# Kernel optimization log

Measured on AMD Instinct MI355X. Metric: run time of the kernel, lower is better.

The kernel has to match this reference:

```python
import jax, jax.numpy as jnp
import numpy as np

H = 128
NG, NS, NP = 50000, 20000, 30000
NUM_PC_FEATURES = 5
EPS = 1e-12


def seg_sum(x, idx, n):
    return jax.ops.segment_sum(x, idx, num_segments=n)


def seg_mean(x, idx, n):
    s = seg_sum(x, idx, n)
    cnt = seg_sum(jnp.ones((x.shape[0],), x.dtype), idx, n)
    return s / jnp.maximum(cnt, 1.0)[:, None]


def gcn_norm(row, col, n, add_self_loops):
    deg = seg_sum(jnp.ones(row.shape, jnp.float32), col, n)
    if add_self_loops:
        deg = deg + 1.0
    dinv = jnp.where(deg > 0, deg ** -0.5, 0.0)
    return dinv[row] * dinv[col], dinv


def tag_conv(x, row, col, n, Ws, b):
    # TAGConv: out = sum_k (A_hat^k x) W_k + b, symmetric norm, no self loops
    norm, _ = gcn_norm(row, col, n, False)
    out = x @ Ws[0]
    h = x
    for k in range(1, Ws.shape[0]):
        h = seg_sum(norm[:, None] * h[row], col, n)
        out = out + h @ Ws[k]
    return out + b


def rgcn_conv(x, row, col, etype, n, W, root, b):
    # RGCNConv: per-relation mean aggregation + root transform
    h = jnp.einsum('nc,rcd->rnd', x, W)  # [R, N, H]
    msg = h[etype, row]                  # [E, H]
    cnt = jnp.zeros((n, W.shape[0]), x.dtype).at[col, etype].add(1.0)
    w = 1.0 / jnp.maximum(cnt[col, etype], 1.0)
    return seg_sum(msg * w[:, None], col, n) + x @ root + b


def gcn_layer(x, row, col, n, W, b):
    # GCNConv: self loops + symmetric normalization
    xW = x @ W
    norm, dinv = gcn_norm(row, col, n, True)
    return seg_sum(norm[:, None] * xW[row], col, n) + (dinv ** 2)[:, None] * xW + b


def sage_conv(xs, xd, row, col, nd, lw, lb, rw):
    # SAGEConv with mean aggregation, root weight, L2 output normalization
    m = seg_mean(xs[row], col, nd)
    out = m @ lw + lb + xd @ rw
    nrm = jnp.maximum(jnp.linalg.norm(out, axis=-1, keepdims=True), EPS)
    return out / nrm


def setup_inputs() -> dict:
    key = jax.random.key(0)
    ks = iter(jax.random.split(key, 64))

    def nrm(shape):
        return jax.random.normal(next(ks), shape, jnp.float32) * 0.05

    def edges(ns, nd, e):
        return jnp.stack([jax.random.randint(next(ks), (e,), 0, ns, jnp.int32),
                          jax.random.randint(next(ks), (e,), 0, nd, jnp.int32)])

    return dict(
        game_x=nrm((NG, 7)),
        state_x=nrm((NS, 6)),
        pc_x=nrm((NP, NUM_PC_FEATURES)),
        edge_index_v_v=edges(NG, NG, 500000),
        edge_type_v_v=jax.random.randint(next(ks), (500000,), 0, 3, jnp.int32),
        edge_index_history_v_s=edges(NG, NS, 300000),
        edge_attr_history_v_s=nrm((300000, 2)),
        edge_index_in_v_s=edges(NG, NS, 300000),
        edge_index_s_s=edges(NS, NS, 200000),
        edge_index_pc_pc=edges(NP, NP, 300000),
        edge_index_pc_state=edges(NP, NS, 200000),
        edge_index_state_pc=edges(NS, NP, 100000),
        tag10_w=nrm((4, 7, H)), tag10_b=nrm((H,)),
        rgcn_w=nrm((3, H, H)), rgcn_root=nrm((H, H)), rgcn_b=nrm((H,)),
        gcn1_w=nrm((NUM_PC_FEATURES, H)), gcn1_b=nrm((H,)),
        gcn2_w=nrm((H, H)), gcn2_b=nrm((H,)),
        rg_key_w=nrm((6, H)), rg_key_b=nrm((H,)),
        rg_query_w=nrm((H, H)), rg_query_b=nrm((H,)),
        rg_value_w=nrm((H, H)), rg_value_b=nrm((H,)),
        rg_edge_w=nrm((2, H)), rg_skip_w=nrm((6, H)), rg_b=nrm((H,)),
        sage32_lw=nrm((H, H)), sage32_lb=nrm((H,)), sage32_rw=nrm((H, H)),
        sage4_lw=nrm((H, H)), sage4_lb=nrm((H,)), sage4_rw=nrm((H, H)),
        sage42_lw=nrm((H, H)), sage42_lb=nrm((H,)), sage42_rw=nrm((H, H)),
        pcs_lw=nrm((H, H)), pcs_lb=nrm((H,)), pcs_rw=nrm((H, H)),
        tag2_w=nrm((3, H, H)), tag2_b=nrm((H,)),
        sage5_lw=nrm((H, H)), sage5_lb=nrm((H,)), sage5_rw=nrm((H, H)),
        lin_w=nrm((H, 32)), lin_b=nrm((32,)),
        linl_w=nrm((32, 1)), linl_b=nrm((1,)),
    )


def reference(game_x, state_x, pc_x, edge_index_v_v, edge_type_v_v,
              edge_index_history_v_s, edge_attr_history_v_s, edge_index_in_v_s,
              edge_index_s_s, edge_index_pc_pc, edge_index_pc_state, edge_index_state_pc,
              tag10_w, tag10_b, rgcn_w, rgcn_root, rgcn_b,
              gcn1_w, gcn1_b, gcn2_w, gcn2_b,
              rg_key_w, rg_key_b, rg_query_w, rg_query_b, rg_value_w, rg_value_b,
              rg_edge_w, rg_skip_w, rg_b,
              sage32_lw, sage32_lb, sage32_rw,
              sage4_lw, sage4_lb, sage4_rw,
              sage42_lw, sage42_lb, sage42_rw,
              pcs_lw, pcs_lb, pcs_rw,
              tag2_w, tag2_b,
              sage5_lw, sage5_lb, sage5_rw,
              lin_w, lin_b, linl_w, linl_b):
    relu = jax.nn.relu
    rvv, cvv = edge_index_v_v[0], edge_index_v_v[1]
    g = relu(tag_conv(game_x, rvv, cvv, NG, tag10_w, tag10_b))
    g = relu(rgcn_conv(g, rvv, cvv, edge_type_v_v, NG, rgcn_w, rgcn_root, rgcn_b))
    rp, cp = edge_index_pc_pc[0], edge_index_pc_pc[1]
    p = relu(gcn_layer(pc_x, rp, cp, NP, gcn1_w, gcn1_b))
    p = relu(gcn_layer(p, rp, cp, NP, gcn2_w, gcn2_b))
    rh, ch = edge_index_history_v_s[0], edge_index_history_v_s[1]
    # ResGatedGraphConv((game, state), H, edge_dim=2)
    kk = state_x @ rg_key_w + rg_key_b
    q = g @ rg_query_w + rg_query_b
    v = g @ rg_value_w + rg_value_b
    e = edge_attr_history_v_s @ rg_edge_w
    eta = jax.nn.sigmoid(kk[ch] + q[rh] + e)
    s = relu(seg_sum(eta * v[rh], ch, NS) + state_x @ rg_skip_w + rg_b)
    s = relu(sage_conv(g, s, rh, ch, NS, sage32_lw, sage32_lb, sage32_rw))
    ri, ci = edge_index_in_v_s[0], edge_index_in_v_s[1]
    s = relu(sage_conv(g, s, ri, ci, NS, sage4_lw, sage4_lb, sage4_rw))
    s = relu(sage_conv(g, s, ri, ci, NS, sage42_lw, sage42_lb, sage42_rw))
    rps, cps = edge_index_pc_state[0], edge_index_pc_state[1]
    s = relu(sage_conv(p, s, rps, cps, NS, pcs_lw, pcs_lb, pcs_rw))
    rs, cs = edge_index_s_s[0], edge_index_s_s[1]
    s = relu(tag_conv(s, rs, cs, NS, tag2_w, tag2_b))
    s = relu(sage_conv(s, s, rs, cs, NS, sage5_lw, sage5_lb, sage5_rw))
    s = relu(s @ lin_w + lin_b)
    return jax.nn.log_softmax(s @ linl_w + linl_b, axis=0)
```

## Files before the change

kernel.cpp:

```cpp
#include <hip/hip_runtime.h>
#include <cstdint>

#define H 128
static const int NG = 50000, NS = 20000, NP = 30000;

#define TG_RELU 2
#define TG_NORM 4
#define TG_OUTBF16 8

#define CSR_CHUNK 8192

typedef __attribute__((ext_vector_type(8))) short bf16x8;
typedef __attribute__((ext_vector_type(4))) float f32x4;

static inline int nblk(long long n) { return (int)((n + 255) / 256); }

__device__ inline unsigned short f2b(float f) {
  unsigned int u = __float_as_uint(f);
  u += 0x7FFFu + ((u >> 16) & 1u);
  return (unsigned short)(u >> 16);
}
__device__ inline float b2f(unsigned short u) {
  return __uint_as_float(((unsigned int)u) << 16);
}

struct Seg6 {
  const int* col[6];
  const int* row[6];
  const int* et0;
  int nodeoff[7];
  int edgeoff[7];
  int mode[6];
  float addself[6];
  int hasdinv[6];
};

__global__ __launch_bounds__(256) void k_hist(Seg6 sg, int EE, int* __restrict__ table) {
  __shared__ int h[512];
  int tid = threadIdx.x, blk = blockIdx.x;
  h[tid] = 0; h[tid + 256] = 0;
  __syncthreads();
  int e0 = blk * CSR_CHUNK, e1 = min(EE, e0 + CSR_CHUNK);
  for (int e = e0 + tid; e < e1; e += 256) {
    int gi = 0;
    while (e >= sg.edgeoff[gi + 1]) gi++;
    int le = e - sg.edgeoff[gi];
    int gn = sg.nodeoff[gi] + sg.col[gi][le];
    atomicAdd(&h[gn >> 9], 1);
  }
  __syncthreads();
  table[blk * 512 + tid] = h[tid];
  table[blk * 512 + tid + 256] = h[tid + 256];
}

__global__ void k_scanT(int* __restrict__ table, int nblkA, int* __restrict__ coarseOff) {
  int b = threadIdx.x;
  int s = 0;
  for (int k = 0; k < nblkA; k++) s += table[k * 512 + b];
  __shared__ int cs[512];
  cs[b] = s;
  __syncthreads();
  for (int off = 1; off < 512; off <<= 1) {
    int v = cs[b];
    int u = (b >= off) ? cs[b - off] : 0;
    __syncthreads();
    cs[b] = v + u;
    __syncthreads();
  }
  int excl = (b > 0) ? cs[b - 1] : 0;
  coarseOff[b] = excl;
  if (b == 511) coarseOff[512] = cs[511];
  int run = excl;
  for (int k = 0; k < nblkA; k++) {
    int t = table[k * 512 + b];
    table[k * 512 + b] = run;
    run += t;
  }
}

__global__ __launch_bounds__(256) void k_scatterA(Seg6 sg, int EE, const int* __restrict__ table,
                                                  uint2* __restrict__ tmp) {
  __shared__ int cur[512];
  int tid = threadIdx.x, blk = blockIdx.x;
  cur[tid] = table[blk * 512 + tid];
  cur[tid + 256] = table[blk * 512 + tid + 256];
  __syncthreads();
  int e0 = blk * CSR_CHUNK, e1 = min(EE, e0 + CSR_CHUNK);
  for (int e = e0 + tid; e < e1; e += 256) {
    int gi = 0;
    while (e >= sg.edgeoff[gi + 1]) gi++;
    int le = e - sg.edgeoff[gi];
    int gn = sg.nodeoff[gi] + sg.col[gi][le];
    int m = sg.mode[gi];
    int pay;
    if (m == 2) pay = le;
    else {
      pay = sg.row[gi][le];
      if (m == 1) pay |= sg.et0[le] << 16;
    }
    int pos = atomicAdd(&cur[gn >> 9], 1);
    tmp[pos] = make_uint2((unsigned)gn, (unsigned)pay);
  }
}

__global__ __launch_bounds__(256) void k_localCSR(const uint2* __restrict__ tmp,
                                                  const int* __restrict__ coarseOff,
                                                  Seg6 sg, int NN, int EE, int B,
                                                  int* __restrict__ rowptr,
                                                  int* __restrict__ eidx,
                                                  float* __restrict__ dinv) {
  int b = blockIdx.x, tid = threadIdx.x;
  int base = b * 512;
  int nNodes = min(512, NN - base);
  int beg = coarseOff[b], end = coarseOff[b + 1];
  __shared__ int cnt[512];
  __shared__ int off[512];
  __shared__ int ps[256];
  cnt[tid] = 0; cnt[tid + 256] = 0;
  __syncthreads();
  for (int j = beg + tid; j < end; j += 256)
    atomicAdd(&cnt[tmp[j].x - base], 1);
  __syncthreads();
  int a = cnt[2 * tid], bb = cnt[2 * tid + 1];
  ps[tid] = a + bb;
  __syncthreads();
  for (int o = 1; o < 256; o <<= 1) {
    int v = ps[tid];
    int u = (tid >= o) ? ps[tid - o] : 0;
    __syncthreads();
    ps[tid] = v + u;
    __syncthreads();
  }
  int excl = (tid > 0) ? ps[tid - 1] : 0;
  off[2 * tid] = excl;
  off[2 * tid + 1] = excl + a;
  __syncthreads();
  for (int i = tid; i < nNodes; i += 256) {
    int gid = base + i;
    rowptr[gid] = beg + off[i];
    int gi = 0;
    while (gid >= sg.nodeoff[gi + 1]) gi++;
    if (sg.hasdinv[gi]) {
      float d = (float)cnt[i] + sg.addself[gi];
      dinv[gid] = (d > 0.f) ? rsqrtf(d) : 0.f;
    }
  }
  if (b == B - 1 && tid == 0) rowptr[NN] = EE;
  __syncthreads();
  for (int j = beg + tid; j < end; j += 256) {
    uint2 p = tmp[j];
    int pos = beg + atomicAdd(&off[p.x - base], 1);
    eidx[pos] = (int)p.y;
  }
}

struct PackD { const float* src; int Ksrc; int Kdst; };
struct Pack17 { PackD d[17]; int koff[18]; };

__global__ void k_pack(Pack17 p, unsigned short* __restrict__ Wt, int totalRows) {
  int t = blockIdx.x * blockDim.x + threadIdx.x;
  if (t >= totalRows * 128) return;
  int gk = t >> 7, n = t & 127;
  int w = 0;
  while (gk >= p.koff[w + 1]) w++;
  int k = gk - p.koff[w];
  float v = (k < p.d[w].Ksrc) ? p.d[w].src[(size_t)k * 128 + n] : 0.f;
  Wt[(size_t)p.koff[w] * 128 + (size_t)n * p.d[w].Kdst + k] = f2b(v);
}

__global__ void k_gather_mean(const unsigned short* __restrict__ src, const int* __restrict__ eidx,
                              const int* __restrict__ rowptr, const int* __restrict__ remap,
                              unsigned short* __restrict__ out) {
  int c = blockIdx.x, h = threadIdx.x;
  int beg = rowptr[c], end = rowptr[c + 1];
  __shared__ int si[128];
  float acc = 0.f;
  for (int j0 = beg; j0 < end; j0 += 128) {
    int nn = min(128, end - j0);
    __syncthreads();
    if (h < nn) {
      int e = eidx[j0 + h];
      si[h] = remap ? remap[e] : e;
    }
    __syncthreads();
    int t = 0;
    for (; t + 4 <= nn; t += 4) {
      float a0 = b2f(src[(size_t)si[t] * H + h]);
      float a1 = b2f(src[(size_t)si[t + 1] * H + h]);
      float a2 = b2f(src[(size_t)si[t + 2] * H + h]);
      float a3 = b2f(src[(size_t)si[t + 3] * H + h]);
      acc += (a0 + a1) + (a2 + a3);
    }
    for (; t < nn; t++) acc += b2f(src[(size_t)si[t] * H + h]);
  }
  int cnt = end - beg;
  out[(size_t)c * H + h] = f2b(acc * (1.f / (float)(cnt > 0 ? cnt : 1)));
}

__global__ void k_gather_rel3(const unsigned short* __restrict__ src, const int* __restrict__ eidx,
                              const int* __restrict__ rowptr, unsigned short* __restrict__ G3) {
  int c = blockIdx.x, h = threadIdx.x;
  int beg = rowptr[c], end = rowptr[c + 1];
  __shared__ int si[128];
  float a0 = 0.f, a1 = 0.f, a2 = 0.f;
  int c0 = 0, c1 = 0, c2 = 0;
  for (int j0 = beg; j0 < end; j0 += 128) {
    int nn = min(128, end - j0);
    __syncthreads();
    if (h < nn) si[h] = eidx[j0 + h];
    __syncthreads();
    for (int t = 0; t < nn; t++) {
      int pk = si[t];
      int rel = pk >> 16;
      float val = b2f(src[(size_t)(pk & 0xFFFF) * H + h]);
      if (rel == 0) { a0 += val; c0++; }
      else if (rel == 1) { a1 += val; c1++; }
      else { a2 += val; c2++; }
    }
  }
  size_t base = (size_t)c * 384;
  G3[base + h] = f2b(a0 * (1.f / (float)(c0 > 0 ? c0 : 1)));
  G3[base + 128 + h] = f2b(a1 * (1.f / (float)(c1 > 0 ? c1 : 1)));
  G3[base + 256 + h] = f2b(a2 * (1.f / (float)(c2 > 0 ? c2 : 1)));
}

__global__ void k_gather_norm(const unsigned short* __restrict__ src, int ldS, int offS,
                              const int* __restrict__ eidx, const int* __restrict__ rowptr,
                              const float* __restrict__ dinv, const unsigned short* __restrict__ selfX,
                              const float* __restrict__ bias, unsigned short* __restrict__ out,
                              int ldD, int offD, int relu) {
  int c = blockIdx.x, h = threadIdx.x;
  int beg = rowptr[c], end = rowptr[c + 1];
  __shared__ int si[128];
  __shared__ float sw[128];
  float acc = 0.f;
  for (int j0 = beg; j0 < end; j0 += 128) {
    int nn = min(128, end - j0);
    __syncthreads();
    if (h < nn) {
      int r = eidx[j0 + h];
      si[h] = r;
      sw[h] = dinv[r];
    }
    __syncthreads();
    int t = 0;
    for (; t + 4 <= nn; t += 4) {
      float a0 = sw[t] * b2f(src[(size_t)si[t] * ldS + offS + h]);
      float a1 = sw[t + 1] * b2f(src[(size_t)si[t + 1] * ldS + offS + h]);
      float a2 = sw[t + 2] * b2f(src[(size_t)si[t + 2] * ldS + offS + h]);
      float a3 = sw[t + 3] * b2f(src[(size_t)si[t + 3] * ldS + offS + h]);
      acc += (a0 + a1) + (a2 + a3);
    }
    for (; t < nn; t++) acc += sw[t] * b2f(src[(size_t)si[t] * ldS + offS + h]);
  }
  float dc = dinv[c];
  float o = acc * dc;
  if (selfX) o += dc * dc * b2f(selfX[(size_t)c * H + h]);
  if (bias) o += bias[h];
  if (relu) o = fmaxf(o, 0.f);
  out[(size_t)c * ldD + offD + h] = f2b(o);
}

__global__ void k_gather_norm7(const unsigned short* __restrict__ src, int ldS, int offS,
                               const int* __restrict__ eidx, const int* __restrict__ rowptr,
                               const float* __restrict__ dinv, unsigned short* __restrict__ dst,
                               int ldD, int offD) {
  int c = blockIdx.x;
  int t = threadIdx.x;
  int f = t & 7, j = t >> 3;
  int beg = rowptr[c], end = rowptr[c + 1];
  __shared__ int si[64];
  __shared__ float sw[64];
  __shared__ float red[8][8];
  float acc = 0.f;
  for (int j0 = beg; j0 < end; j0 += 64) {
    int nn = min(64, end - j0);
    __syncthreads();
    if (t < nn) {
      int r = eidx[j0 + t] & 0xFFFF;
      si[t] = r;
      sw[t] = dinv[r];
    }
    __syncthreads();
    if (f < 7)
      for (int u = j; u < nn; u += 8) acc += sw[u] * b2f(src[(size_t)si[u] * ldS + offS + f]);
  }
  red[j][f] = acc;
  __syncthreads();
  if (j == 0 && f < 7) {
    float s = 0.f;
    for (int u = 0; u < 8; u++) s += red[u][f];
    dst[(size_t)c * ldD + offD + f] = f2b(s * dinv[c]);
  }
}

__global__ void k_resgated_gather(const unsigned short* __restrict__ kk,
                                  const unsigned short* __restrict__ q,
                                  const unsigned short* __restrict__ v,
                                  const float* __restrict__ ea,
                                  const float* __restrict__ We, const int* __restrict__ rh,
                                  const int* __restrict__ eidx, const int* __restrict__ rowptr,
                                  const float* __restrict__ sx, const float* __restrict__ Wsk,
                                  const float* __restrict__ rgb, unsigned short* __restrict__ out) {
  int c = blockIdx.x, h = threadIdx.x;
  int beg = rowptr[c], end = rowptr[c + 1];
  __shared__ int sr[64];
  __shared__ float se0[64], se1[64];
  float kload = b2f(kk[(size_t)c * H + h]);
  float we0 = We[h], we1 = We[H + h];
  float acc = 0.f;
  for (int j0 = beg; j0 < end; j0 += 64) {
    int nn = min(64, end - j0);
    __syncthreads();
    if (h < nn) {
      int e = eidx[j0 + h];
      sr[h] = rh[e];
      se0[h] = ea[2 * e];
      se1[h] = ea[2 * e + 1];
    }
    __syncthreads();
    for (int t = 0; t < nn; t++) {
      int r = sr[t];
      float x = kload + b2f(q[(size_t)r * H + h]) + se0[t] * we0 + se1[t] * we1;
      float eta = 1.f / (1.f + __expf(-x));
      acc += eta * b2f(v[(size_t)r * H + h]);
    }
  }
  float skip = rgb[h];
#pragma unroll
  for (int f = 0; f < 6; f++) skip = fmaf(sx[c * 6 + f], Wsk[f * H + h], skip);
  out[(size_t)c * H + h] = f2b(fmaxf(acc + skip, 0.f));
}

__global__ void k_copy7b(const float* __restrict__ src, unsigned short* __restrict__ dst, int n) {
  long long t = (long long)blockIdx.x * blockDim.x + threadIdx.x;
  int i = (int)(t >> 3), f = (int)(t & 7);
  if (i < n && f < 7) dst[(size_t)i * 32 + f] = f2b(src[(size_t)i * 7 + f]);
}

__global__ void k_gemm128b(const float* __restrict__ X, const float* __restrict__ W,
                           const float* __restrict__ b, unsigned short* __restrict__ out,
                           int M, int K) {
  long long t = (long long)blockIdx.x * blockDim.x + threadIdx.x;
  if (t >= (long long)M * H) return;
  int i = (int)(t >> 7), h = (int)(t & 127);
  float acc = b ? b[h] : 0.f;
  const float* x = X + (long long)i * K;
  for (int k = 0; k < K; k++) acc = fmaf(x[k], W[k * H + h], acc);
  out[t] = f2b(acc);
}

__global__ __launch_bounds__(256) void k_mgemm(const unsigned short* __restrict__ X1, int ldX1, int K1,
                                               const unsigned short* __restrict__ W1t,
                                               const unsigned short* __restrict__ X2, int ldX2, int K2,
                                               const unsigned short* __restrict__ W2t,
                                               const float* __restrict__ bias,
                                               void* __restrict__ Cv, long ldC,
                                               int M, int flags) {
  __shared__ unsigned short Als[64 * 40];
  __shared__ unsigned short Bls[128 * 40];
  __shared__ float rs[2][64];
  int tid = threadIdx.x;
  int lane = tid & 63, wv = tid >> 6;
  int m = lane & 15, q = lane >> 4;
  int rbase = (wv & 1) * 32;
  int cbase = (wv >> 1) * 64;
  int blockRow = blockIdx.x * 64;
  int sr = tid >> 2, skc = (tid & 3) * 8;
  f32x4 acc[2][4];
#pragma unroll
  for (int a = 0; a < 2; a++)
#pragma unroll
    for (int b = 0; b < 4; b++) acc[a][b] = (f32x4){0.f, 0.f, 0.f, 0.f};

  int Ktot = K1 + K2;
  for (int k0 = 0; k0 < Ktot; k0 += 32) {
    const unsigned short* Xb;
    const unsigned short* Wt_;
    int kr, ldx, Kw;
    if (k0 < K1) { Xb = X1; Wt_ = W1t; kr = k0; ldx = ldX1; Kw = K1; }
    else { Xb = X2; Wt_ = W2t; kr = k0 - K1; ldx = ldX2; Kw = K2; }
    __syncthreads();
    {
      int gr = blockRow + sr;
      bf16x8 xv = (bf16x8){0, 0, 0, 0, 0, 0, 0, 0};
      if (gr < M) xv = *(const bf16x8*)(Xb + (size_t)gr * ldx + kr + skc);
      *(bf16x8*)&Als[sr * 40 + skc] = xv;
    }
#pragma unroll
    for (int it = 0; it < 2; it++) {
      int fid = it * 256 + tid;
      int n = fid >> 2, kc = (fid & 3) * 8;
      *(bf16x8*)&Bls[n * 40 + kc] = *(const bf16x8*)(Wt_ + (size_t)n * Kw + kr + kc);
    }
    __syncthreads();
    bf16x8 a0 = *(const bf16x8*)&Als[(rbase + m) * 40 + q * 8];
    bf16x8 a1 = *(const bf16x8*)&Als[(rbase + 16 + m) * 40 + q * 8];
    bf16x8 b0 = *(const bf16x8*)&Bls[(cbase + m) * 40 + q * 8];
    bf16x8 b1 = *(const bf16x8*)&Bls[(cbase + 16 + m) * 40 + q * 8];
    bf16x8 b2 = *(const bf16x8*)&Bls[(cbase + 32 + m) * 40 + q * 8];
    bf16x8 b3 = *(const bf16x8*)&Bls[(cbase + 48 + m) * 40 + q * 8];
    acc[0][0] = __builtin_amdgcn_mfma_f32_16x16x32_bf16(a0, b0, acc[0][0], 0, 0, 0);
    acc[0][1] = __builtin_amdgcn_mfma_f32_16x16x32_bf16(a0, b1, acc[0][1], 0, 0, 0);
    acc[0][2] = __builtin_amdgcn_mfma_f32_16x16x32_bf16(a0, b2, acc[0][2], 0, 0, 0);
    acc[0][3] = __builtin_amdgcn_mfma_f32_16x16x32_bf16(a0, b3, acc[0][3], 0, 0, 0);
    acc[1][0] = __builtin_amdgcn_mfma_f32_16x16x32_bf16(a1, b0, acc[1][0], 0, 0, 0);
    acc[1][1] = __builtin_amdgcn_mfma_f32_16x16x32_bf16(a1, b1, acc[1][1], 0, 0, 0);
    acc[1][2] = __builtin_amdgcn_mfma_f32_16x16x32_bf16(a1, b2, acc[1][2], 0, 0, 0);
    acc[1][3] = __builtin_amdgcn_mfma_f32_16x16x32_bf16(a1, b3, acc[1][3], 0, 0, 0);
  }
  float ov[2][4][4];
  float bcol[4] = {0.f, 0.f, 0.f, 0.f};
  if (bias) {
#pragma unroll
    for (int j = 0; j < 4; j++) bcol[j] = bias[cbase + j * 16 + m];
  }
#pragma unroll
  for (int a = 0; a < 2; a++)
#pragma unroll
    for (int j = 0; j < 4; j++)
#pragma unroll
      for (int i = 0; i < 4; i++) ov[a][j][i] = acc[a][j][i] + bcol[j];

  if (flags & TG_NORM) {
#pragma unroll
    for (int a = 0; a < 2; a++)
#pragma unroll
      for (int i = 0; i < 4; i++) {
        float p = 0.f;
#pragma unroll
        for (int j = 0; j < 4; j++) p = fmaf(ov[a][j][i], ov[a][j][i], p);
        p += __shfl_xor(p, 1);
        p += __shfl_xor(p, 2);
        p += __shfl_xor(p, 4);
        p += __shfl_xor(p, 8);
        if (m == 0) rs[wv >> 1][rbase + a * 16 + q * 4 + i] = p;
      }
    __syncthreads();
#pragma unroll
    for (int a = 0; a < 2; a++)
#pragma unroll
      for (int i = 0; i < 4; i++) {
        int ridx = rbase + a * 16 + q * 4 + i;
        float s = rs[0][ridx] + rs[1][ridx];
        float f = 1.f / fmaxf(sqrtf(s), 1e-12f);
#pragma unroll
        for (int j = 0; j < 4; j++) ov[a][j][i] = fmaxf(ov[a][j][i] * f, 0.f);
      }
  } else if (flags & TG_RELU) {
#pragma unroll
    for (int a = 0; a < 2; a++)
#pragma unroll
      for (int j = 0; j < 4; j++)
#pragma unroll
        for (int i = 0; i < 4; i++) ov[a][j][i] = fmaxf(ov[a][j][i], 0.f);
  }
  if (flags & TG_OUTBF16) {
    unsigned short* C = (unsigned short*)Cv;
#pragma unroll
    for (int a = 0; a < 2; a++)
#pragma unroll
      for (int i = 0; i < 4; i++) {
        int row = blockRow + rbase + a * 16 + q * 4 + i;
        if (row < M) {
#pragma unroll
          for (int j = 0; j < 4; j++)
            C[(size_t)row * ldC + cbase + j * 16 + m] = f2b(ov[a][j][i]);
        }
      }
  } else {
    float* C = (float*)Cv;
#pragma unroll
    for (int a = 0; a < 2; a++)
#pragma unroll
      for (int i = 0; i < 4; i++) {
        int row = blockRow + rbase + a * 16 + q * 4 + i;
        if (row < M) {
#pragma unroll
          for (int j = 0; j < 4; j++)
            C[(size_t)row * ldC + cbase + j * 16 + m] = ov[a][j][i];
        }
      }
  }
}

static inline int mgb(int M) { return (M + 63) / 64; }

__global__ __launch_bounds__(256) void k_head(const float* __restrict__ X,
                                              const float* __restrict__ lw,
                                              const float* __restrict__ lb,
                                              const float* __restrict__ lwl,
                                              const float* __restrict__ lbl,
                                              float* __restrict__ z, int M) {
  __shared__ float Wl[128 * 32];
  __shared__ float Xs[8][128];
  int tid = threadIdx.x;
  for (int i = tid * 4; i < 4096; i += 1024) *(float4*)&Wl[i] = *(const float4*)&lw[i];
  int rowBase = blockIdx.x * 8;
  {
    int idx = tid * 4;
    int xr = idx >> 7, xc = idx & 127;
    int grow = rowBase + xr;
    float4 v = make_float4(0.f, 0.f, 0.f, 0.f);
    if (grow < M) v = *(const float4*)(X + (size_t)grow * H + xc);
    *(float4*)&Xs[xr][xc] = v;
  }
  __syncthreads();
  int r = tid >> 5, o = tid & 31;
  float acc = lb[o];
  for (int k = 0; k < 128; k++) acc = fmaf(Xs[r][k], Wl[k * 32 + o], acc);
  acc = fmaxf(acc, 0.f) * lwl[o];
  for (int s = 16; s > 0; s >>= 1) acc += __shfl_down(acc, s, 32);
  int grow = rowBase + r;
  if (o == 0 && grow < M) z[grow] = acc + lbl[0];
}

__global__ void k_logsoftmax(const float* __restrict__ z, float* __restrict__ out, int n) {
  __shared__ float red[256];
  int tid = threadIdx.x;
  float m = -1e30f;
  for (int i = tid; i < n; i += 256) m = fmaxf(m, z[i]);
  red[tid] = m;
  __syncthreads();
  for (int s = 128; s > 0; s >>= 1) {
    if (tid < s) red[tid] = fmaxf(red[tid], red[tid + s]);
    __syncthreads();
  }
  float mx = red[0];
  __syncthreads();
  float sum = 0.f;
  for (int i = tid; i < n; i += 256) sum += __expf(z[i] - mx);
  red[tid] = sum;
  __syncthreads();
  for (int s = 128; s > 0; s >>= 1) {
    if (tid < s) red[tid] += red[tid + s];
    __syncthreads();
  }
  float lse = mx + logf(red[0]);
  for (int i = tid; i < n; i += 256) out[i] = z[i] - lse;
}

extern "C" void kernel_launch(void* const* d_in, const int* in_sizes, int n_in,
                              void* d_out, int out_size, void* d_ws, size_t ws_size,
                              hipStream_t stream) {
  const float* game_x = (const float*)d_in[0];
  const float* state_x = (const float*)d_in[1];
  const float* pc_x = (const float*)d_in[2];
  const int* ei_vv = (const int*)d_in[3];
  const int* et_vv = (const int*)d_in[4];
  const int* ei_hist = (const int*)d_in[5];
  const float* ea_hist = (const float*)d_in[6];
  const int* ei_in = (const int*)d_in[7];
  const int* ei_ss = (const int*)d_in[8];
  const int* ei_pp = (const int*)d_in[9];
  const int* ei_ps = (const int*)d_in[10];
  const float* tag10_w = (const float*)d_in[12];
  const float* tag10_b = (const float*)d_in[13];
  const float* rgcn_w = (const float*)d_in[14];
  const float* rgcn_root = (const float*)d_in[15];
  const float* rgcn_b = (const float*)d_in[16];
  const float* gcn1_w = (const float*)d_in[17];
  const float* gcn1_b = (const float*)d_in[18];
  const float* gcn2_w = (const float*)d_in[19];
  const float* gcn2_b = (const float*)d_in[20];
  const float* rg_key_w = (const float*)d_in[21];
  const float* rg_key_b = (const float*)d_in[22];
  const float* rg_query_w = (const float*)d_in[23];
  const float* rg_query_b = (const float*)d_in[24];
  const float* rg_value_w = (const float*)d_in[25];
  const float* rg_value_b = (const float*)d_in[26];
  const float* rg_edge_w = (const float*)d_in[27];
  const float* rg_skip_w = (const float*)d_in[28];
  const float* rg_b = (const float*)d_in[29];
  const float* sage32_lw = (const float*)d_in[30];
  const float* sage32_lb = (const float*)d_in[31];
  const float* sage32_rw = (const float*)d_in[32];
  const float* sage4_lw = (const float*)d_in[33];
  const float* sage4_lb = (const float*)d_in[34];
  const float* sage4_rw = (const float*)d_in[35];
  const float* sage42_lw = (const float*)d_in[36];
  const float* sage42_lb = (const float*)d_in[37];
  const float* sage42_rw = (const float*)d_in[38];
  const float* pcs_lw = (const float*)d_in[39];
  const float* pcs_lb = (const float*)d_in[40];
  const float* pcs_rw = (const float*)d_in[41];
  const float* tag2_w = (const float*)d_in[42];
  const float* tag2_b = (const float*)d_in[43];
  const float* sage5_lw = (const float*)d_in[44];
  const float* sage5_lb = (const float*)d_in[45];
  const float* sage5_rw = (const float*)d_in[46];
  const float* lin_w = (const float*)d_in[47];
  const float* lin_b = (const float*)d_in[48];
  const float* linl_w = (const float*)d_in[49];
  const float* linl_b = (const float*)d_in[50];

  const int Evv = in_sizes[3] / 2, Eh = in_sizes[5] / 2, Ein = in_sizes[7] / 2,
            Ess = in_sizes[8] / 2, Epp = in_sizes[9] / 2, Eps = in_sizes[10] / 2;
  const int EE = Evv + Epp + Eh + Ein + Eps + Ess;
  const int NN = NG + NP + 4 * NS;

  char* base = (char*)d_ws;
  const size_t B_NGH = (size_t)NG * H * 2;
  const size_t B_NPH = (size_t)NP * H * 2;
  const size_t B_NSH = (size_t)NS * H * 2;
  unsigned short* g_tag_b = (unsigned short*)base;
  unsigned short* g_b = (unsigned short*)(base + B_NGH);
  char* C0 = base + 2 * B_NGH;
  uint2* tmp_pairs = (uint2*)C0;
  unsigned short* P_tag10_b = (unsigned short*)C0;
  unsigned short* G3_b = (unsigned short*)C0;
  unsigned short* xW_b = (unsigned short*)C0;
  unsigned short* p1b_b = (unsigned short*)(C0 + B_NPH);
  unsigned short* p2b_b = (unsigned short*)(C0 + 2 * B_NPH);
  unsigned short* v_b = (unsigned short*)C0;
  unsigned short* q_b = g_tag_b;
  unsigned short* P_tag2_b = (unsigned short*)C0;
  char* S0 = base + 2 * B_NGH + 46000000;
  unsigned short* S_a_b = (unsigned short*)S0;
  unsigned short* S_b_b = (unsigned short*)(S0 + B_NSH);
  unsigned short* m_buf_b = (unsigned short*)(S0 + 2 * B_NSH);
  unsigned short* kk_b = (unsigned short*)(S0 + 3 * B_NSH);
  float* Sfin = (float*)(S0 + 4 * B_NSH);
  unsigned short* Wt = (unsigned short*)(S0 + 4 * B_NSH + (size_t)NS * H * 4);
  int* ip = (int*)(S0 + 4 * B_NSH + (size_t)NS * H * 4 + 700000);
  int* rp_all = ip; ip += NN + 1;
  int* eidx_all = ip; ip += EE;
  int* table = ip; ip += 512 * 240;
  int* coarseOff = ip; ip += 520;
  float* fp = (float*)ip;
  float* dinv_all = fp; fp += NN;
  float* z = fp; fp += NS;

  Seg6 sg;
  sg.col[0] = ei_vv + Evv;  sg.row[0] = ei_vv;
  sg.col[1] = ei_pp + Epp;  sg.row[1] = ei_pp;
  sg.col[2] = ei_hist + Eh; sg.row[2] = ei_hist;
  sg.col[3] = ei_in + Ein;  sg.row[3] = ei_in;
  sg.col[4] = ei_ps + Eps;  sg.row[4] = ei_ps;
  sg.col[5] = ei_ss + Ess;  sg.row[5] = ei_ss;
  sg.et0 = et_vv;
  int no[7] = {0, NG, NG + NP, NG + NP + NS, NG + NP + 2 * NS, NG + NP + 3 * NS, NN};
  int eo[7] = {0, Evv, Evv + Epp, Evv + Epp + Eh, Evv + Epp + Eh + Ein,
               Evv + Epp + Eh + Ein + Eps, EE};
  for (int i = 0; i < 7; i++) { sg.nodeoff[i] = no[i]; sg.edgeoff[i] = eo[i]; }
  int md[6] = {1, 0, 2, 0, 0, 0};
  float as[6] = {0.f, 1.f, 0.f, 0.f, 0.f, 0.f};
  int hd[6] = {1, 1, 0, 0, 0, 1};
  for (int i = 0; i < 6; i++) { sg.mode[i] = md[i]; sg.addself[i] = as[i]; sg.hasdinv[i] = hd[i]; }

  const int* rp_vv = rp_all + no[0];
  const int* rp_pp = rp_all + no[1];
  const int* rp_hh = rp_all + no[2];
  const int* rp_in = rp_all + no[3];
  const int* rp_ps = rp_all + no[4];
  const int* rp_ss = rp_all + no[5];
  const float* dinvG = dinv_all + no[0];
  const float* dinvP = dinv_all + no[1];
  const float* dinvS = dinv_all + no[5];
  const int* rh = ei_hist;

  Pack17 pk;
  const float* wsrc[17] = {tag10_w, rgcn_w, rgcn_root, gcn2_w, rg_query_w, rg_value_w,
                           sage32_lw, sage32_rw, sage4_lw, sage4_rw, sage42_lw, sage42_rw,
                           pcs_lw, pcs_rw, tag2_w, sage5_lw, sage5_rw};
  int ksrc[17] = {28, 384, 128, 128, 128, 128, 128, 128, 128, 128, 128, 128, 128, 128, 384, 128, 128};
  int kdst[17] = {32, 384, 128, 128, 128, 128, 128, 128, 128, 128, 128, 128, 128, 128, 384, 128, 128};
  int run = 0;
  for (int i = 0; i < 17; i++) {
    pk.d[i].src = wsrc[i]; pk.d[i].Ksrc = ksrc[i]; pk.d[i].Kdst = kdst[i];
    pk.koff[i] = run; run += kdst[i];
  }
  pk.koff[17] = run;
  unsigned short* WT[17];
  for (int i = 0; i < 17; i++) WT[i] = Wt + (size_t)pk.koff[i] * 128;
  k_pack<<<nblk((long long)run * 128), 256, 0, stream>>>(pk, Wt, run);

  int nblkA = (EE + CSR_CHUNK - 1) / CSR_CHUNK;
  int B = (NN + 511) / 512;
  k_hist<<<nblkA, 256, 0, stream>>>(sg, EE, table);
  k_scanT<<<1, 512, 0, stream>>>(table, nblkA, coarseOff);
  k_scatterA<<<nblkA, 256, 0, stream>>>(sg, EE, table, tmp_pairs);
  k_localCSR<<<B, 256, 0, stream>>>(tmp_pairs, coarseOff, sg, NN, EE, B,
                                    rp_all, eidx_all, dinv_all);

  hipMemsetAsync(P_tag10_b, 0, (size_t)NG * 32 * 2, stream);
  k_copy7b<<<nblk((long long)NG * 8), 256, 0, stream>>>(game_x, P_tag10_b, NG);
  k_gather_norm7<<<NG, 64, 0, stream>>>(P_tag10_b, 32, 0, eidx_all, rp_vv, dinvG, P_tag10_b, 32, 7);
  k_gather_norm7<<<NG, 64, 0, stream>>>(P_tag10_b, 32, 7, eidx_all, rp_vv, dinvG, P_tag10_b, 32, 14);
  k_gather_norm7<<<NG, 64, 0, stream>>>(P_tag10_b, 32, 14, eidx_all, rp_vv, dinvG, P_tag10_b, 32, 21);
  k_mgemm<<<mgb(NG), 256, 0, stream>>>(P_tag10_b, 32, 32, WT[0], nullptr, 0, 0, nullptr,
                                       tag10_b, g_tag_b, H, NG, TG_RELU | TG_OUTBF16);

  k_gather_rel3<<<NG, 128, 0, stream>>>(g_tag_b, eidx_all, rp_vv, G3_b);
  k_mgemm<<<mgb(NG), 256, 0, stream>>>(G3_b, 384, 384, WT[1], g_tag_b, H, H, WT[2],
                                       rgcn_b, g_b, H, NG, TG_RELU | TG_OUTBF16);

  k_gemm128b<<<nblk((long long)NP * H), 256, 0, stream>>>(pc_x, gcn1_w, nullptr, xW_b, NP, 5);
  k_gather_norm<<<NP, 128, 0, stream>>>(xW_b, H, 0, eidx_all, rp_pp, dinvP, xW_b, gcn1_b,
                                        p1b_b, H, 0, 1);
  k_mgemm<<<mgb(NP), 256, 0, stream>>>(p1b_b, H, H, WT[3], nullptr, 0, 0, nullptr,
                                       nullptr, xW_b, H, NP, TG_OUTBF16);
  k_gather_norm<<<NP, 128, 0, stream>>>(xW_b, H, 0, eidx_all, rp_pp, dinvP, xW_b, gcn2_b,
                                        p2b_b, H, 0, 1);

  k_gemm128b<<<nblk((long long)NS * H), 256, 0, stream>>>(state_x, rg_key_w, rg_key_b, kk_b, NS, 6);
  k_mgemm<<<mgb(NG), 256, 0, stream>>>(g_b, H, H, WT[4], nullptr, 0, 0, nullptr,
                                       rg_query_b, q_b, H, NG, TG_OUTBF16);
  k_mgemm<<<mgb(NG), 256, 0, stream>>>(g_b, H, H, WT[5], nullptr, 0, 0, nullptr,
                                       rg_value_b, v_b, H, NG, TG_OUTBF16);
  k_resgated_gather<<<NS, 128, 0, stream>>>(kk_b, q_b, v_b, ea_hist, rg_edge_w, rh,
                                            eidx_all, rp_hh, state_x, rg_skip_w, rg_b, S_a_b);

  k_gather_mean<<<NS, 128, 0, stream>>>(g_b, eidx_all, rp_hh, rh, m_buf_b);
  k_mgemm<<<mgb(NS), 256, 0, stream>>>(m_buf_b, H, H, WT[6], S_a_b, H, H, WT[7],
                                       sage32_lb, S_b_b, H, NS, TG_NORM | TG_OUTBF16);

  k_gather_mean<<<NS, 128, 0, stream>>>(g_b, eidx_all, rp_in, nullptr, m_buf_b);
  k_mgemm<<<mgb(NS), 256, 0, stream>>>(m_buf_b, H, H, WT[8], S_b_b, H, H, WT[9],
                                       sage4_lb, S_a_b, H, NS, TG_NORM | TG_OUTBF16);
  k_mgemm<<<mgb(NS), 256, 0, stream>>>(m_buf_b, H, H, WT[10], S_a_b, H, H, WT[11],
                                       sage42_lb, S_b_b, H, NS, TG_NORM | TG_OUTBF16);

  k_gather_mean<<<NS, 128, 0, stream>>>(p2b_b, eidx_all, rp_ps, nullptr, m_buf_b);
  k_mgemm<<<mgb(NS), 256, 0, stream>>>(m_buf_b, H, H, WT[12], S_b_b, H, H, WT[13],
                                       pcs_lb, P_tag2_b, 384, NS, TG_NORM | TG_OUTBF16);

  k_gather_norm<<<NS, 128, 0, stream>>>(P_tag2_b, 384, 0, eidx_all, rp_ss, dinvS, nullptr,
                                        nullptr, P_tag2_b, 384, 128, 0);
  k_gather_norm<<<NS, 128, 0, stream>>>(P_tag2_b, 384, 128, eidx_all, rp_ss, dinvS, nullptr,
                                        nullptr, P_tag2_b, 384, 256, 0);
  k_mgemm<<<mgb(NS), 256, 0, stream>>>(P_tag2_b, 384, 384, WT[14], nullptr, 0, 0, nullptr,
                                       tag2_b, S_b_b, H, NS, TG_RELU | TG_OUTBF16);

  k_gather_mean<<<NS, 128, 0, stream>>>(S_b_b, eidx_all, rp_ss, nullptr, m_buf_b);
  k_mgemm<<<mgb(NS), 256, 0, stream>>>(m_buf_b, H, H, WT[15], S_b_b, H, H, WT[16],
                                       sage5_lb, Sfin, H, NS, TG_NORM);

  k_head<<<(NS + 7) / 8, 256, 0, stream>>>(Sfin, lin_w, lin_b, linl_w, linl_b, z, NS);
  k_logsoftmax<<<1, 256, 0, stream>>>(z, (float*)d_out, NS);
}
```

Measured before the change: 805.1 us.

## Rewrite CSR gather kernels as wave-per-node with paired bf16 loads

```diff
diff --git a/kernel.cpp b/kernel.cpp
--- a/kernel.cpp
+++ b/kernel.cpp
@@ -22,6 +22,12 @@
 }
 __device__ inline float b2f(unsigned short u) {
   return __uint_as_float(((unsigned int)u) << 16);
+}
+__device__ inline float2 bfp2(unsigned int u) {
+  return make_float2(__uint_as_float(u << 16), __uint_as_float(u & 0xFFFF0000u));
+}
+__device__ inline unsigned int f2bfp(float x, float y) {
+  return ((unsigned int)f2b(y) << 16) | (unsigned int)f2b(x);
 }
 
 struct Seg6 {
@@ -168,97 +174,165 @@
   Wt[(size_t)p.koff[w] * 128 + (size_t)n * p.d[w].Kdst + k] = f2b(v);
 }
 
-__global__ void k_gather_mean(const unsigned short* __restrict__ src, const int* __restrict__ eidx,
-                              const int* __restrict__ rowptr, const int* __restrict__ remap,
-                              unsigned short* __restrict__ out) {
-  int c = blockIdx.x, h = threadIdx.x;
+__global__ __launch_bounds__(256) void k_gmean(const unsigned short* __restrict__ src,
+                                               const int* __restrict__ eidx,
+                                               const int* __restrict__ rowptr,
+                                               unsigned short* __restrict__ out, int N) {
+  int c = blockIdx.x * 4 + (threadIdx.x >> 6);
+  if (c >= N) return;
+  int lane = threadIdx.x & 63;
   int beg = rowptr[c], end = rowptr[c + 1];
-  __shared__ int si[128];
-  float acc = 0.f;
-  for (int j0 = beg; j0 < end; j0 += 128) {
-    int nn = min(128, end - j0);
-    __syncthreads();
-    if (h < nn) {
-      int e = eidx[j0 + h];
-      si[h] = remap ? remap[e] : e;
-    }
-    __syncthreads();
-    int t = 0;
-    for (; t + 4 <= nn; t += 4) {
-      float a0 = b2f(src[(size_t)si[t] * H + h]);
-      float a1 = b2f(src[(size_t)si[t + 1] * H + h]);
-      float a2 = b2f(src[(size_t)si[t + 2] * H + h]);
-      float a3 = b2f(src[(size_t)si[t + 3] * H + h]);
-      acc += (a0 + a1) + (a2 + a3);
-    }
-    for (; t < nn; t++) acc += b2f(src[(size_t)si[t] * H + h]);
+  float2 A0 = {0.f, 0.f}, A1 = {0.f, 0.f}, A2 = {0.f, 0.f}, A3 = {0.f, 0.f};
+  int j = beg;
+  for (; j + 4 <= end; j += 4) {
+    int e0 = eidx[j], e1 = eidx[j + 1], e2 = eidx[j + 2], e3 = eidx[j + 3];
+    unsigned int r0 = *(const unsigned int*)(src + (size_t)e0 * H + lane * 2);
+    unsigned int r1 = *(const unsigned int*)(src + (size_t)e1 * H + lane * 2);
+    unsigned int r2 = *(const unsigned int*)(src + (size_t)e2 * H + lane * 2);
+    unsigned int r3 = *(const unsigned int*)(src + (size_t)e3 * H + lane * 2);
+    float2 v0 = bfp2(r0), v1 = bfp2(r1), v2 = bfp2(r2), v3 = bfp2(r3);
+    A0.x += v0.x; A0.y += v0.y;
+    A1.x += v1.x; A1.y += v1.y;
+    A2.x += v2.x; A2.y += v2.y;
+    A3.x += v3.x; A3.y += v3.y;
+  }
+  for (; j < end; j++) {
+    float2 v = bfp2(*(const unsigned int*)(src + (size_t)eidx[j] * H + lane * 2));
+    A0.x += v.x; A0.y += v.y;
   }
   int cnt = end - beg;
-  out[(size_t)c * H + h] = f2b(acc * (1.f / (float)(cnt > 0 ? cnt : 1)));
-}
-
-__global__ void k_gather_rel3(const unsigned short* __restrict__ src, const int* __restrict__ eidx,
-                              const int* __restrict__ rowptr, unsigned short* __restrict__ G3) {
-  int c = blockIdx.x, h = threadIdx.x;
+  float s = 1.f / (float)(cnt > 0 ? cnt : 1);
+  float ox = (A0.x + A1.x + A2.x + A3.x) * s;
+  float oy = (A0.y + A1.y + A2.y + A3.y) * s;
+  *(unsigned int*)(out + (size_t)c * H + lane * 2) = f2bfp(ox, oy);
+}
+
+__global__ __launch_bounds__(256) void k_grel3(const unsigned short* __restrict__ src,
+                                               const int* __restrict__ eidx,
+                                               const int* __restrict__ rowptr,
+                                               unsigned short* __restrict__ G3, int N) {
+  int c = blockIdx.x * 4 + (threadIdx.x >> 6);
+  if (c >= N) return;
+  int lane = threadIdx.x & 63;
   int beg = rowptr[c], end = rowptr[c + 1];
-  __shared__ int si[128];
-  float a0 = 0.f, a1 = 0.f, a2 = 0.f;
+  float2 a0 = {0.f, 0.f}, a1 = {0.f, 0.f}, a2 = {0.f, 0.f};
   int c0 = 0, c1 = 0, c2 = 0;
-  for (int j0 = beg; j0 < end; j0 += 128) {
-    int nn = min(128, end - j0);
-    __syncthreads();
-    if (h < nn) si[h] = eidx[j0 + h];
-    __syncthreads();
-    for (int t = 0; t < nn; t++) {
-      int pk = si[t];
-      int rel = pk >> 16;
-      float val = b2f(src[(size_t)(pk & 0xFFFF) * H + h]);
-      if (rel == 0) { a0 += val; c0++; }
-      else if (rel == 1) { a1 += val; c1++; }
-      else { a2 += val; c2++; }
-    }
-  }
-  size_t base = (size_t)c * 384;
-  G3[base + h] = f2b(a0 * (1.f / (float)(c0 > 0 ? c0 : 1)));
-  G3[base + 128 + h] = f2b(a1 * (1.f / (float)(c1 > 0 ? c1 : 1)));
-  G3[base + 256 + h] = f2b(a2 * (1.f / (float)(c2 > 0 ? c2 : 1)));
-}
-
-__global__ void k_gather_norm(const unsigned short* __restrict__ src, int ldS, int offS,
-                              const int* __restrict__ eidx, const int* __restrict__ rowptr,
-                              const float* __restrict__ dinv, const unsigned short* __restrict__ selfX,
-                              const float* __restrict__ bias, unsigned short* __restrict__ out,
-                              int ldD, int offD, int relu) {
-  int c = blockIdx.x, h = threadIdx.x;
+  for (int j = beg; j < end; j++) {
+    int pk = eidx[j];
+    int rel = pk >> 16;
+    float2 v = bfp2(*(const unsigned int*)(src + (size_t)(pk & 0xFFFF) * H + lane * 2));
+    if (rel == 0) { a0.x += v.x; a0.y += v.y; c0++; }
+    else if (rel == 1) { a1.x += v.x; a1.y += v.y; c1++; }
+    else { a2.x += v.x; a2.y += v.y; c2++; }
+  }
+  float s0 = 1.f / (float)(c0 > 0 ? c0 : 1);
+  float s1 = 1.f / (float)(c1 > 0 ? c1 : 1);
+  float s2 = 1.f / (float)(c2 > 0 ? c2 : 1);
+  size_t base = (size_t)c * 384 + lane * 2;
+  *(unsigned int*)(G3 + base) = f2bfp(a0.x * s0, a0.y * s0);
+  *(unsigned int*)(G3 + base + 128) = f2bfp(a1.x * s1, a1.y * s1);
+  *(unsigned int*)(G3 + base + 256) = f2bfp(a2.x * s2, a2.y * s2);
+}
+
+__global__ __launch_bounds__(256) void k_gnorm(const unsigned short* __restrict__ src,
+                                               long ldS, int offS,
+                                               const int* __restrict__ eidx,
+                                               const int* __restrict__ rowptr,
+                                               const float* __restrict__ dinv,
+                                               const unsigned short* __restrict__ selfX,
+                                               const float* __restrict__ bias,
+                                               unsigned short* __restrict__ out,
+                                               long ldD, int offD, int relu, int N) {
+  int c = blockIdx.x * 4 + (threadIdx.x >> 6);
+  if (c >= N) return;
+  int lane = threadIdx.x & 63;
   int beg = rowptr[c], end = rowptr[c + 1];
-  __shared__ int si[128];
-  __shared__ float sw[128];
-  float acc = 0.f;
-  for (int j0 = beg; j0 < end; j0 += 128) {
-    int nn = min(128, end - j0);
-    __syncthreads();
-    if (h < nn) {
-      int r = eidx[j0 + h];
-      si[h] = r;
-      sw[h] = dinv[r];
-    }
-    __syncthreads();
-    int t = 0;
-    for (; t + 4 <= nn; t += 4) {
-      float a0 = sw[t] * b2f(src[(size_t)si[t] * ldS + offS + h]);
-      float a1 = sw[t + 1] * b2f(src[(size_t)si[t + 1] * ldS + offS + h]);
-      float a2 = sw[t + 2] * b2f(src[(size_t)si[t + 2] * ldS + offS + h]);
-      float a3 = sw[t + 3] * b2f(src[(size_t)si[t + 3] * ldS + offS + h]);
-      acc += (a0 + a1) + (a2 + a3);
-    }
-    for (; t < nn; t++) acc += sw[t] * b2f(src[(size_t)si[t] * ldS + offS + h]);
+  float2 A0 = {0.f, 0.f}, A1 = {0.f, 0.f}, A2 = {0.f, 0.f}, A3 = {0.f, 0.f};
+  int j = beg;
+  for (; j + 4 <= end; j += 4) {
+    int e0 = eidx[j], e1 = eidx[j + 1], e2 = eidx[j + 2], e3 = eidx[j + 3];
+    float w0 = dinv[e0], w1 = dinv[e1], w2 = dinv[e2], w3 = dinv[e3];
+    float2 v0 = bfp2(*(const unsigned int*)(src + (size_t)e0 * ldS + offS + lane * 2));
+    float2 v1 = bfp2(*(const unsigned int*)(src + (size_t)e1 * ldS + offS + lane * 2));
+    float2 v2 = bfp2(*(const unsigned int*)(src + (size_t)e2 * ldS + offS + lane * 2));
+    float2 v3 = bfp2(*(const unsigned int*)(src + (size_t)e3 * ldS + offS + lane * 2));
+    A0.x = fmaf(w0, v0.x, A0.x); A0.y = fmaf(w0, v0.y, A0.y);
+    A1.x = fmaf(w1, v1.x, A1.x); A1.y = fmaf(w1, v1.y, A1.y);
+    A2.x = fmaf(w2, v2.x, A2.x); A2.y = fmaf(w2, v2.y, A2.y);
+    A3.x = fmaf(w3, v3.x, A3.x); A3.y = fmaf(w3, v3.y, A3.y);
+  }
+  for (; j < end; j++) {
+    int e = eidx[j];
+    float w = dinv[e];
+    float2 v = bfp2(*(const unsigned int*)(src + (size_t)e * ldS + offS + lane * 2));
+    A0.x = fmaf(w, v.x, A0.x); A0.y = fmaf(w, v.y, A0.y);
   }
   float dc = dinv[c];
-  float o = acc * dc;
-  if (selfX) o += dc * dc * b2f(selfX[(size_t)c * H + h]);
-  if (bias) o += bias[h];
-  if (relu) o = fmaxf(o, 0.f);
-  out[(size_t)c * ldD + offD + h] = f2b(o);
+  float ox = (A0.x + A1.x + A2.x + A3.x) * dc;
+  float oy = (A0.y + A1.y + A2.y + A3.y) * dc;
+  if (selfX) {
+    float2 sv = bfp2(*(const unsigned int*)(selfX + (size_t)c * H + lane * 2));
+    ox += dc * dc * sv.x;
+    oy += dc * dc * sv.y;
+  }
+  if (bias) {
+    float2 bv = *(const float2*)(bias + lane * 2);
+    ox += bv.x; oy += bv.y;
+  }
+  if (relu) { ox = fmaxf(ox, 0.f); oy = fmaxf(oy, 0.f); }
+  *(unsigned int*)(out + (size_t)c * ldD + offD + lane * 2) = f2bfp(ox, oy);
+}
+
+__global__ __launch_bounds__(256) void k_resgated_mean(const unsigned short* __restrict__ kk,
+                                                       const unsigned short* __restrict__ q,
+                                                       const unsigned short* __restrict__ v,
+                                                       const unsigned short* __restrict__ g,
+                                                       const float* __restrict__ ea,
+                                                       const float* __restrict__ We,
+                                                       const int* __restrict__ rh,
+                                                       const int* __restrict__ eidx,
+                                                       const int* __restrict__ rowptr,
+                                                       const float* __restrict__ sx,
+                                                       const float* __restrict__ Wsk,
+                                                       const float* __restrict__ rgb,
+                                                       unsigned short* __restrict__ outS,
+                                                       unsigned short* __restrict__ outM, int N) {
+  int c = blockIdx.x * 4 + (threadIdx.x >> 6);
+  if (c >= N) return;
+  int lane = threadIdx.x & 63;
+  int d0 = lane * 2;
+  int beg = rowptr[c], end = rowptr[c + 1];
+  float2 kload = bfp2(*(const unsigned int*)(kk + (size_t)c * H + d0));
+  float2 we0 = make_float2(We[d0], We[d0 + 1]);
+  float2 we1 = make_float2(We[H + d0], We[H + d0 + 1]);
+  float2 accS = {0.f, 0.f}, accM = {0.f, 0.f};
+  for (int j = beg; j < end; j++) {
+    int e = eidx[j];
+    int r = rh[e];
+    float a0 = ea[2 * e], a1 = ea[2 * e + 1];
+    float2 qv = bfp2(*(const unsigned int*)(q + (size_t)r * H + d0));
+    float2 vv = bfp2(*(const unsigned int*)(v + (size_t)r * H + d0));
+    float2 gv = bfp2(*(const unsigned int*)(g + (size_t)r * H + d0));
+    float x0 = kload.x + qv.x + a0 * we0.x + a1 * we1.x;
+    float x1 = kload.y + qv.y + a0 * we0.y + a1 * we1.y;
+    float eta0 = 1.f / (1.f + __expf(-x0));
+    float eta1 = 1.f / (1.f + __expf(-x1));
+    accS.x = fmaf(eta0, vv.x, accS.x);
+    accS.y = fmaf(eta1, vv.y, accS.y);
+    accM.x += gv.x; accM.y += gv.y;
+  }
+  float sk0 = rgb[d0], sk1 = rgb[d0 + 1];
+#pragma unroll
+  for (int f = 0; f < 6; f++) {
+    float xf = sx[c * 6 + f];
+    sk0 = fmaf(xf, Wsk[f * H + d0], sk0);
+    sk1 = fmaf(xf, Wsk[f * H + d0 + 1], sk1);
+  }
+  *(unsigned int*)(outS + (size_t)c * H + d0) =
+      f2bfp(fmaxf(accS.x + sk0, 0.f), fmaxf(accS.y + sk1, 0.f));
+  int cnt = end - beg;
+  float s = 1.f / (float)(cnt > 0 ? cnt : 1);
+  *(unsigned int*)(outM + (size_t)c * H + d0) = f2bfp(accM.x * s, accM.y * s);
 }
 
 __global__ void k_gather_norm7(const unsigned short* __restrict__ src, int ldS, int offS,
@@ -292,44 +366,6 @@
     for (int u = 0; u < 8; u++) s += red[u][f];
     dst[(size_t)c * ldD + offD + f] = f2b(s * dinv[c]);
   }
-}
-
-__global__ void k_resgated_gather(const unsigned short* __restrict__ kk,
-                                  const unsigned short* __restrict__ q,
-                                  const unsigned short* __restrict__ v,
-                                  const float* __restrict__ ea,
-                                  const float* __restrict__ We, const int* __restrict__ rh,
-                                  const int* __restrict__ eidx, const int* __restrict__ rowptr,
-                                  const float* __restrict__ sx, const float* __restrict__ Wsk,
-                                  const float* __restrict__ rgb, unsigned short* __restrict__ out) {
-  int c = blockIdx.x, h = threadIdx.x;
-  int beg = rowptr[c], end = rowptr[c + 1];
-  __shared__ int sr[64];
-  __shared__ float se0[64], se1[64];
-  float kload = b2f(kk[(size_t)c * H + h]);
-  float we0 = We[h], we1 = We[H + h];
-  float acc = 0.f;
-  for (int j0 = beg; j0 < end; j0 += 64) {
-    int nn = min(64, end - j0);
-    __syncthreads();
-    if (h < nn) {
-      int e = eidx[j0 + h];
-      sr[h] = rh[e];
-      se0[h] = ea[2 * e];
-      se1[h] = ea[2 * e + 1];
-    }
-    __syncthreads();
-    for (int t = 0; t < nn; t++) {
-      int r = sr[t];
-      float x = kload + b2f(q[(size_t)r * H + h]) + se0[t] * we0 + se1[t] * we1;
-      float eta = 1.f / (1.f + __expf(-x));
-      acc += eta * b2f(v[(size_t)r * H + h]);
-    }
-  }
-  float skip = rgb[h];
-#pragma unroll
-  for (int f = 0; f < 6; f++) skip = fmaf(sx[c * 6 + f], Wsk[f * H + h], skip);
-  out[(size_t)c * H + h] = f2b(fmaxf(acc + skip, 0.f));
 }
 
 __global__ void k_copy7b(const float* __restrict__ src, unsigned short* __restrict__ dst, int n) {
@@ -691,48 +727,48 @@
   k_mgemm<<<mgb(NG), 256, 0, stream>>>(P_tag10_b, 32, 32, WT[0], nullptr, 0, 0, nullptr,
                                        tag10_b, g_tag_b, H, NG, TG_RELU | TG_OUTBF16);
 
-  k_gather_rel3<<<NG, 128, 0, stream>>>(g_tag_b, eidx_all, rp_vv, G3_b);
+  k_grel3<<<(NG + 3) / 4, 256, 0, stream>>>(g_tag_b, eidx_all, rp_vv, G3_b, NG);
   k_mgemm<<<mgb(NG), 256, 0, stream>>>(G3_b, 384, 384, WT[1], g_tag_b, H, H, WT[2],
                                        rgcn_b, g_b, H, NG, TG_RELU | TG_OUTBF16);
 
   k_gemm128b<<<nblk((long long)NP * H), 256, 0, stream>>>(pc_x, gcn1_w, nullptr, xW_b, NP, 5);
-  k_gather_norm<<<NP, 128, 0, stream>>>(xW_b, H, 0, eidx_all, rp_pp, dinvP, xW_b, gcn1_b,
-                                        p1b_b, H, 0, 1);
+  k_gnorm<<<(NP + 3) / 4, 256, 0, stream>>>(xW_b, H, 0, eidx_all, rp_pp, dinvP, xW_b, gcn1_b,
+                                            p1b_b, H, 0, 1, NP);
   k_mgemm<<<mgb(NP), 256, 0, stream>>>(p1b_b, H, H, WT[3], nullptr, 0, 0, nullptr,
                                        nullptr, xW_b, H, NP, TG_OUTBF16);
-  k_gather_norm<<<NP, 128, 0, stream>>>(xW_b, H, 0, eidx_all, rp_pp, dinvP, xW_b, gcn2_b,
-                                        p2b_b, H, 0, 1);
+  k_gnorm<<<(NP + 3) / 4, 256, 0, stream>>>(xW_b, H, 0, eidx_all, rp_pp, dinvP, xW_b, gcn2_b,
+                                            p2b_b, H, 0, 1, NP);
 
   k_gemm128b<<<nblk((long long)NS * H), 256, 0, stream>>>(state_x, rg_key_w, rg_key_b, kk_b, NS, 6);
   k_mgemm<<<mgb(NG), 256, 0, stream>>>(g_b, H, H, WT[4], nullptr, 0, 0, nullptr,
                                        rg_query_b, q_b, H, NG, TG_OUTBF16);
   k_mgemm<<<mgb(NG), 256, 0, stream>>>(g_b, H, H, WT[5], nullptr, 0, 0, nullptr,
                                        rg_value_b, v_b, H, NG, TG_OUTBF16);
-  k_resgated_gather<<<NS, 128, 0, stream>>>(kk_b, q_b, v_b, ea_hist, rg_edge_w, rh,
-                                            eidx_all, rp_hh, state_x, rg_skip_w, rg_b, S_a_b);
-
-  k_gather_mean<<<NS, 128, 0, stream>>>(g_b, eidx_all, rp_hh, rh, m_buf_b);
+  k_resgated_mean<<<(NS + 3) / 4, 256, 0, stream>>>(kk_b, q_b, v_b, g_b, ea_hist, rg_edge_w, rh,
+                                                    eidx_all, rp_hh, state_x, rg_skip_w, rg_b,
+                                                    S_a_b, m_buf_b, NS);
+
   k_mgemm<<<mgb(NS), 256, 0, stream>>>(m_buf_b, H, H, WT[6], S_a_b, H, H, WT[7],
                                        sage32_lb, S_b_b, H, NS, TG_NORM | TG_OUTBF16);
 
-  k_gather_mean<<<NS, 128, 0, stream>>>(g_b, eidx_all, rp_in, nullptr, m_buf_b);
+  k_gmean<<<(NS + 3) / 4, 256, 0, stream>>>(g_b, eidx_all, rp_in, m_buf_b, NS);
   k_mgemm<<<mgb(NS), 256, 0, stream>>>(m_buf_b, H, H, WT[8], S_b_b, H, H, WT[9],
                                        sage4_lb, S_a_b, H, NS, TG_NORM | TG_OUTBF16);
   k_mgemm<<<mgb(NS), 256, 0, stream>>>(m_buf_b, H, H, WT[10], S_a_b, H, H, WT[11],
                                        sage42_lb, S_b_b, H, NS, TG_NORM | TG_OUTBF16);
 
-  k_gather_mean<<<NS, 128, 0, stream>>>(p2b_b, eidx_all, rp_ps, nullptr, m_buf_b);
+  k_gmean<<<(NS + 3) / 4, 256, 0, stream>>>(p2b_b, eidx_all, rp_ps, m_buf_b, NS);
   k_mgemm<<<mgb(NS), 256, 0, stream>>>(m_buf_b, H, H, WT[12], S_b_b, H, H, WT[13],
                                        pcs_lb, P_tag2_b, 384, NS, TG_NORM | TG_OUTBF16);
 
-  k_gather_norm<<<NS, 128, 0, stream>>>(P_tag2_b, 384, 0, eidx_all, rp_ss, dinvS, nullptr,
-                                        nullptr, P_tag2_b, 384, 128, 0);
-  k_gather_norm<<<NS, 128, 0, stream>>>(P_tag2_b, 384, 128, eidx_all, rp_ss, dinvS, nullptr,
-                                        nullptr, P_tag2_b, 384, 256, 0);
+  k_gnorm<<<(NS + 3) / 4, 256, 0, stream>>>(P_tag2_b, 384, 0, eidx_all, rp_ss, dinvS, nullptr,
+                                            nullptr, P_tag2_b, 384, 128, 0, NS);
+  k_gnorm<<<(NS + 3) / 4, 256, 0, stream>>>(P_tag2_b, 384, 128, eidx_all, rp_ss, dinvS, nullptr,
+                                            nullptr, P_tag2_b, 384, 256, 0, NS);
   k_mgemm<<<mgb(NS), 256, 0, stream>>>(P_tag2_b, 384, 384, WT[14], nullptr, 0, 0, nullptr,
                                        tag2_b, S_b_b, H, NS, TG_RELU | TG_OUTBF16);
 
-  k_gather_mean<<<NS, 128, 0, stream>>>(S_b_b, eidx_all, rp_ss, nullptr, m_buf_b);
+  k_gmean<<<(NS + 3) / 4, 256, 0, stream>>>(S_b_b, eidx_all, rp_ss, m_buf_b, NS);
   k_mgemm<<<mgb(NS), 256, 0, stream>>>(m_buf_b, H, H, WT[15], S_b_b, H, H, WT[16],
                                        sage5_lb, Sfin, H, NS, TG_NORM);
 
```

Result: no change. 800.2 us (-0.6%).
